# Optimization experiments

Hardware: AMD Instinct MI355X
Metric: run time of the kernel (lower is better)

Reference implementation:

```python
import jax, jax.numpy as jnp
import numpy as np

MODEL_DIM = 1024
HIDDEN = 2048
NUM_GROUPS = 2
EXPERTS_PER_GP = 4
NUM_EXPERTS = NUM_GROUPS * EXPERTS_PER_GP
TOP_K = 2
B, T = 2, 2048


def _swiglu(x):
    a, b = jnp.split(x, 2, axis=-1)
    return jax.nn.silu(a) * b


def setup_inputs() -> dict:
    key = jax.random.key(0)
    ks = jax.random.split(key, 7)
    s = 0.02  # init scale
    return {
        "x": jax.random.normal(ks[0], (B, T, MODEL_DIM), jnp.float32),
        # torch Linear weight layout [out_features, in_features]
        "w_in": jax.random.normal(ks[1], (HIDDEN * 2, MODEL_DIM), jnp.float32) * s,   # shared_in
        "w_out": jax.random.normal(ks[2], (MODEL_DIM, HIDDEN), jnp.float32) * s,      # shared_out
        "w1": jax.random.normal(ks[3], (HIDDEN * 2, MODEL_DIM), jnp.float32) * s,     # w1_shared
        "w2": jax.random.normal(ks[4], (NUM_EXPERTS, MODEL_DIM, HIDDEN), jnp.float32) * s,  # w2_expert stack
        "wg": jax.random.normal(ks[5], (NUM_GROUPS, MODEL_DIM), jnp.float32) * s,     # group_gate
        "we": jax.random.normal(ks[6], (NUM_EXPERTS, MODEL_DIM), jnp.float32) * s,    # expert_gate
        "gb": jnp.zeros((NUM_GROUPS,), jnp.float32),   # group_bias
        "eb": jnp.zeros((NUM_EXPERTS,), jnp.float32),  # expert_bias
    }


def reference(x, w_in, w_out, w1, w2, wg, we, gb, eb):
    Bs, Ts, C = x.shape
    S = Bs * Ts
    flat = x.reshape(S, C)

    # shared expert path
    shared = _swiglu(flat @ w_in.T) @ w_out.T                    # [S, C]

    # level-1: group gate (top-1)
    g_probs = jax.nn.softmax(flat @ wg.T + gb, axis=-1)          # [S, G]
    g_idx = jnp.argmax(g_probs, axis=-1)                         # [S]

    # level-2: expert gate masked to the chosen group
    e_logits = flat @ we.T + eb                                  # [S, E]
    egid = jnp.arange(NUM_EXPERTS) // EXPERTS_PER_GP             # expert -> group id
    masked = jnp.where(g_idx[:, None] == egid[None, :], e_logits, -jnp.inf)
    e_probs = jax.nn.softmax(masked, axis=-1)                    # zero outside group

    g_prob = jnp.take_along_axis(g_probs, g_idx[:, None], axis=1)  # [S, 1]
    p_expert = e_probs * g_prob                                  # [S, E]

    topv, topi = jax.lax.top_k(p_expert, TOP_K)                  # [S, k]

    # per-token per-expert combine weight (dense [S, E], rows k-sparse)
    w_se = jnp.zeros((S, NUM_EXPERTS), x.dtype).at[
        jnp.arange(S)[:, None], topi].add(topv)

    # w1 is shared across experts -> compute hidden once for all tokens
    h = _swiglu(flat @ w1.T)                                     # [S, H]

    # routed = sum_e w_se[:, e] * (h @ w2[e].T); scale commutes through linear
    routed = jnp.zeros_like(shared)
    for e in range(NUM_EXPERTS):  # small fixed expert count
        routed = routed + (h * w_se[:, e:e + 1]) @ w2[e].T

    return (shared + routed).reshape(Bs, Ts, C)
```

## Files before the change

### kernel.cpp

```cpp
#include <hip/hip_runtime.h>
#include <math.h>


#define C_DIM 1024
#define H_DIM 2048
#define S_TOK 4096

typedef _Float16 f16x8 __attribute__((ext_vector_type(8)));
typedef float f32x4 __attribute__((ext_vector_type(4)));

#define AS3(p) ((__attribute__((address_space(3))) void*)(p))
#define AS1c(p) ((const __attribute__((address_space(1))) void*)(p))

__global__ __launch_bounds__(256) void cvt_all(
    const float* __restrict__ x, const float* __restrict__ w_in,
    const float* __restrict__ w1, const float* __restrict__ w_out,
    const float* __restrict__ w2, _Float16* __restrict__ xh,
    _Float16* __restrict__ wprime, _Float16* __restrict__ wouth,
    _Float16* __restrict__ w2h) {
  int i = blockIdx.x * 256 + threadIdx.x;
  const float* s; _Float16* d; size_t soff, doff;
  if (i < 524288) { s = x; d = xh; soff = doff = (size_t)i; }
  else if (i < 1572864) {
    int n = i - 524288;
    int out_row = n >> 7, kc = n & 127;
    int wmat = out_row >> 12, r = out_row & 4095;
    int g = r >> 5, ii = r & 31;
    int src_row = (ii < 16) ? (g * 16 + ii) : (2048 + g * 16 + (ii - 16));
    s = wmat ? w1 : w_in; d = wprime;
    soff = (size_t)src_row * 128 + kc;
    doff = (size_t)n;
  } else if (i < 1835008) { int n = i - 1572864; s = w_out; d = wouth; soff = doff = (size_t)n; }
  else { int n = i - 1835008; s = w2; d = w2h; soff = doff = (size_t)n; }
  const float4* sp = reinterpret_cast<const float4*>(s) + soff * 2;
  float4 a = sp[0], b = sp[1];
  f16x8 h;
  h[0] = (_Float16)a.x; h[1] = (_Float16)a.y; h[2] = (_Float16)a.z; h[3] = (_Float16)a.w;
  h[4] = (_Float16)b.x; h[5] = (_Float16)b.y; h[6] = (_Float16)b.z; h[7] = (_Float16)b.w;
  reinterpret_cast<f16x8*>(d)[doff] = h;
}

__global__ __launch_bounds__(256) void gate_kernel(const float* __restrict__ x,
    const float* __restrict__ wg, const float* __restrict__ we,
    const float* __restrict__ gb, const float* __restrict__ eb,
    int* __restrict__ top2_e, float* __restrict__ top2_w) {
  const int lane = threadIdx.x & 63;
  const int token = blockIdx.x * 4 + (threadIdx.x >> 6);
  const float* xr = x + (size_t)token * C_DIM + lane * 16;
  float xv[16];
#pragma unroll
  for (int i = 0; i < 16; i += 4) {
    float4 t = *reinterpret_cast<const float4*>(xr + i);
    xv[i] = t.x; xv[i + 1] = t.y; xv[i + 2] = t.z; xv[i + 3] = t.w;
  }
  float dots[10];
#pragma unroll
  for (int g = 0; g < 10; ++g) {
    const float* wr = (g < 2 ? wg + (size_t)g * C_DIM : we + (size_t)(g - 2) * C_DIM) + lane * 16;
    float d = 0.f;
#pragma unroll
    for (int i = 0; i < 16; i += 4) {
      float4 t = *reinterpret_cast<const float4*>(wr + i);
      d += xv[i] * t.x + xv[i + 1] * t.y + xv[i + 2] * t.z + xv[i + 3] * t.w;
    }
#pragma unroll
    for (int off = 32; off > 0; off >>= 1) d += __shfl_xor(d, off);
    dots[g] = d;
  }
  if (lane != 0) return;
  float g0 = dots[0] + gb[0], g1 = dots[1] + gb[1];
  int gidx = (g0 >= g1) ? 0 : 1;
  float gm = fmaxf(g0, g1);
  float ex0 = expf(g0 - gm), ex1 = expf(g1 - gm);
  float gprob = (gidx == 0 ? ex0 : ex1) / (ex0 + ex1);
  const int base = gidx * 4;
  float el[4];
  float m = -1e30f;
#pragma unroll
  for (int jj = 0; jj < 4; ++jj) { el[jj] = dots[2 + base + jj] + eb[base + jj]; m = fmaxf(m, el[jj]); }
  float s = 0.f;
#pragma unroll
  for (int jj = 0; jj < 4; ++jj) { el[jj] = expf(el[jj] - m); s += el[jj]; }
  float p[8];
#pragma unroll
  for (int e = 0; e < 8; ++e) p[e] = 0.f;
#pragma unroll
  for (int jj = 0; jj < 4; ++jj) p[base + jj] = el[jj] / s * gprob;
  int i1 = 0; float v1 = -1.f;
#pragma unroll
  for (int e = 0; e < 8; ++e) if (p[e] > v1) { v1 = p[e]; i1 = e; }
  int i2 = -1; float v2 = -1.f;
#pragma unroll
  for (int e = 0; e < 8; ++e) if (e != i1 && p[e] > v2) { v2 = p[e]; i2 = e; }
  top2_e[token * 2] = i1;     top2_w[token * 2] = v1;
  top2_e[token * 2 + 1] = i2; top2_w[token * 2 + 1] = v2;
}

__global__ __launch_bounds__(256) void scanfill(const int* __restrict__ top2_e,
    const float* __restrict__ top2_w, int* __restrict__ offs_g,
    int* __restrict__ tok_list, float* __restrict__ scale_list,
    int* __restrict__ tok2slot) {
  __shared__ int cnt[8], offs[9], cur[8];
  const int tid = threadIdx.x;
  if (tid < 8) { cnt[tid] = 0; cur[tid] = 0; }
  __syncthreads();
  for (int i = tid; i < 2 * S_TOK; i += 256) atomicAdd(&cnt[top2_e[i]], 1);
  __syncthreads();
  if (tid == 0) {
    offs[0] = 0;
    for (int e = 0; e < 8; ++e) offs[e + 1] = offs[e] + cnt[e];
    for (int e = 0; e < 9; ++e) offs_g[e] = offs[e];
  }
  __syncthreads();
  for (int i = tid; i < 2 * S_TOK; i += 256) {
    int e = top2_e[i];
    int slot = atomicAdd(&cur[e], 1);
    int g = offs[e] + slot;
    tok_list[g] = i >> 1;
    scale_list[g] = top2_w[i];
    tok2slot[i] = g;
  }
}

__device__ __forceinline__ void stage_tile(_Float16* lds_, const _Float16* src,
                                           int ld, int tid) {
#pragma unroll
  for (int i = 0; i < 2; ++i) {
    int c = tid + i * 512;
    int row = c >> 3;
    int u = c & 7;
    const _Float16* g = src + (size_t)row * ld + ((u ^ (row & 7)) << 3);
    _Float16* l = lds_ + ((c & ~63) << 3);
    __builtin_amdgcn_global_load_lds(AS1c(g), AS3(l), 16, 0, 0);
  }
}

__device__ __forceinline__ f16x8 frag_ld(const _Float16* t, int row, int u) {
  return *reinterpret_cast<const f16x8*>(t + row * 64 + ((u ^ (row & 7)) << 3));
}

#define BAR __builtin_amdgcn_s_barrier()
#define LGKM0 do { asm volatile("s_waitcnt lgkmcnt(0)" ::: "memory"); \
                   __builtin_amdgcn_sched_barrier(0); } while (0)
#define PRI1 __builtin_amdgcn_s_setprio(1)
#define PRI0 __builtin_amdgcn_s_setprio(0)

#define STAGEA(h_, t_) do { \
  const _Float16* s_ = aS[h_] + (size_t)(t_) * 64; \
  _Float16* d_ = lds + ((t_) & 1) * 32768 + (h_) * 8192 + grp0; \
  __builtin_amdgcn_global_load_lds(AS1c(s_), AS3(d_), 16, 0, 0); \
  __builtin_amdgcn_global_load_lds(AS1c(s_ + 65536), AS3(d_ + 4096), 16, 0, 0); \
} while (0)
#define STAGEB(h_, t_) do { \
  const _Float16* s_ = bS[h_] + (size_t)(t_) * 64; \
  _Float16* d_ = lds + ((t_) & 1) * 32768 + 16384 + (h_) * 8192 + grp0; \
  __builtin_amdgcn_global_load_lds(AS1c(s_), AS3(d_), 16, 0, 0); \
  __builtin_amdgcn_global_load_lds(AS1c(s_ + 65536), AS3(d_ + 4096), 16, 0, 0); \
} while (0)

#define LDA(MB_) do { _Pragma("unroll") for (int mm = 0; mm < 4; ++mm) \
  { _Pragma("unroll") for (int ks = 0; ks < 2; ++ks) \
    af[mm][ks] = frag_ld(At, wm * 128 + (MB_) + mm * 16 + lr, ks * 4 + lq); } } while (0)
#define LDB(DST_, CB_) do { _Pragma("unroll") for (int nn = 0; nn < 2; ++nn) \
  { _Pragma("unroll") for (int ks = 0; ks < 2; ++ks) \
    DST_[nn][ks] = frag_ld(Bt, wn * 64 + (CB_) + nn * 16 + lr, ks * 4 + lq); } } while (0)
#define QUAD(MB_, BF_, NB_) do { \
  _Pragma("unroll") for (int ks = 0; ks < 2; ++ks) \
  _Pragma("unroll") for (int mm = 0; mm < 4; ++mm) \
  _Pragma("unroll") for (int nn = 0; nn < 2; ++nn) \
    acc[(MB_) + mm][(NB_) + nn] = __builtin_amdgcn_mfma_f32_16x16x32_f16( \
        af[mm][ks], BF_[nn][ks], acc[(MB_) + mm][(NB_) + nn], 0, 0, 0); \
} while (0)

__global__ __launch_bounds__(512, 2) void gemm_fused_swiglu(
    const _Float16* __restrict__ A, const _Float16* __restrict__ Wp,
    _Float16* __restrict__ H1, _Float16* __restrict__ H2) {
  __shared__ _Float16 lds[65536];
  const int tid = threadIdx.x;
  const int lane = tid & 63;
  const int wid = tid >> 6;
  const int wm = wid >> 2, wn = wid & 3;
  const int lr = lane & 15, lq = lane >> 4;

  const int bid = blockIdx.x;
  const int xcd = bid & 7, j = bid >> 3;
  const int nb = xcd * 4 + (j & 3);
  const int mb = j >> 2;
  const int row0 = mb * 256;
  const int colg0 = nb * 256;

  const int rA = tid >> 3, uA = tid & 7;
  const int grp0 = (tid & ~63) << 3;
  const int swz = (uA ^ (rA & 7)) << 3;
  const _Float16* aS[2];
  const _Float16* bS[2];
#pragma unroll
  for (int h = 0; h < 2; ++h) {
    aS[h] = A  + (size_t)(row0  + h * 128 + rA) * 1024 + swz;
    bS[h] = Wp + (size_t)(colg0 + h * 128 + rA) * 1024 + swz;
  }

  STAGEB(0, 0); STAGEB(1, 0); STAGEA(0, 0); STAGEA(1, 0);
  STAGEB(0, 1); STAGEB(1, 1); STAGEA(0, 1); STAGEA(1, 1);
  asm volatile("s_waitcnt vmcnt(8)" ::: "memory");
  BAR;

  f32x4 acc[8][4] = {};
  f16x8 af[4][2], bf[2][2], bf2[2][2];

  for (int t = 0; t < 16; ++t) {
    const _Float16* At = lds + (t & 1) * 32768;
    const _Float16* Bt = At + 16384;
    LDA(0); LDB(bf, 0);
    BAR; LGKM0; PRI1; QUAD(0, bf, 0); PRI0; BAR;
    LDB(bf2, 32);
    BAR; LGKM0; PRI1; QUAD(0, bf2, 2); PRI0; BAR;
    LDA(64);
    if (t < 14) { STAGEB(0, t + 2); STAGEB(1, t + 2); }
    BAR; LGKM0; PRI1; QUAD(4, bf, 0); PRI0; BAR;
    if (t < 14) { STAGEA(0, t + 2); STAGEA(1, t + 2); }
    BAR; PRI1; QUAD(4, bf2, 2); PRI0;
    if (t <= 13) { asm volatile("s_waitcnt vmcnt(8)" ::: "memory"); }
    else if (t == 14) { asm volatile("s_waitcnt vmcnt(0)" ::: "memory"); }
    BAR;
  }

  _Float16* Hd = (colg0 >= 4096) ? H2 : H1;
  const int col0 = colg0 & 4095;
  const int hbase = (col0 >> 1) + wn * 32 + lr;
#pragma unroll
  for (int mm = 0; mm < 8; ++mm)
#pragma unroll
    for (int np = 0; np < 2; ++np)
#pragma unroll
      for (int r = 0; r < 4; ++r) {
        float a = acc[mm][np * 2][r];
        float b = acc[mm][np * 2 + 1][r];
        float h = (a / (1.0f + expf(-a))) * b;
        int row = row0 + wm * 128 + mm * 16 + lq * 4 + r;
        Hd[(size_t)row * H_DIM + hbase + np * 16] = (_Float16)h;
      }
}

__global__ __launch_bounds__(512) void gemm_out(
    const _Float16* __restrict__ H1, const _Float16* __restrict__ H2,
    const _Float16* __restrict__ Wout, const _Float16* __restrict__ W2,
    const int* __restrict__ offs_g, const int* __restrict__ tok_list,
    const float* __restrict__ scale_list,
    float* __restrict__ out, _Float16* __restrict__ routed) {
  __shared__ _Float16 At[128 * 64];
  __shared__ _Float16 Bt[128 * 64];
  __shared__ float sse[128];
  const int tid = threadIdx.x;
  const int lane = tid & 63;
  const int wid = tid >> 6;
  const int wm = wid >> 2, wn = wid & 3;

  const int b = blockIdx.x;
  const bool shared_role = (b < 256);
  int rb, cb, offs_e = 0, n_e = 0;
  const _Float16* Bp;
  if (shared_role) {
    int x = b & 7, k = b >> 3;
    rb = x + (k >> 3) * 8; cb = k & 7;
    Bp = Wout;
  } else {
    int bp = b - 256;
    int e = bp & 7, k = bp >> 3;
    rb = k >> 3; cb = k & 7;
    offs_e = offs_g[e]; n_e = offs_g[e + 1] - offs_e;
    if (rb * 128 >= n_e) return;
    Bp = W2 + (size_t)e * C_DIM * H_DIM;
    if (tid < 128) {
      int lrr = rb * 128 + tid;
      sse[tid] = (lrr < n_e) ? scale_list[offs_e + lrr] : 0.f;
    }
  }

  const _Float16* aptr[2];
  _Float16* ldst[2];
#pragma unroll
  for (int i = 0; i < 2; ++i) {
    int c = tid + i * 512;
    int row = c >> 3, u = c & 7;
    int swz = (u ^ (row & 7)) << 3;
    const _Float16* rowbase;
    if (shared_role) {
      rowbase = H1 + (size_t)(rb * 128 + row) * H_DIM;
    } else {
      int lrr = rb * 128 + row;
      int gs = offs_e + (lrr < n_e ? lrr : n_e - 1);
      rowbase = H2 + (size_t)tok_list[gs] * H_DIM;
    }
    aptr[i] = rowbase + swz;
    ldst[i] = At + ((c & ~63) << 3);
  }

  f32x4 acc[4][2] = {};
  for (int kt = 0; kt < H_DIM; kt += 64) {
#pragma unroll
    for (int i = 0; i < 2; ++i)
      __builtin_amdgcn_global_load_lds(AS1c(aptr[i] + kt), AS3(ldst[i]), 16, 0, 0);
    stage_tile(Bt, Bp + (size_t)cb * 128 * H_DIM + kt, H_DIM, tid);
    __syncthreads();
#pragma unroll
    for (int ks = 0; ks < 2; ++ks) {
      const int u = (ks << 2) + (lane >> 4);
      f16x8 af[4], bfr[2];
#pragma unroll
      for (int m = 0; m < 4; ++m)
        af[m] = frag_ld(At, wm * 64 + m * 16 + (lane & 15), u);
#pragma unroll
      for (int n = 0; n < 2; ++n)
        bfr[n] = frag_ld(Bt, wn * 32 + n * 16 + (lane & 15), u);
#pragma unroll
      for (int m = 0; m < 4; ++m)
#pragma unroll
        for (int n = 0; n < 2; ++n)
          acc[m][n] = __builtin_amdgcn_mfma_f32_16x16x32_f16(af[m], bfr[n], acc[m][n], 0, 0, 0);
    }
    __syncthreads();
  }

#pragma unroll
  for (int m = 0; m < 4; ++m)
#pragma unroll
    for (int n = 0; n < 2; ++n)
#pragma unroll
      for (int r = 0; r < 4; ++r) {
        int rloc = wm * 64 + m * 16 + ((lane >> 4) << 2) + r;
        int col = cb * 128 + wn * 32 + n * 16 + (lane & 15);
        if (shared_role) {
          out[(size_t)(rb * 128 + rloc) * C_DIM + col] = acc[m][n][r];
        } else {
          int lrr = rb * 128 + rloc;
          if (lrr < n_e)
            routed[(size_t)(offs_e + lrr) * C_DIM + col] =
                (_Float16)(sse[rloc] * acc[m][n][r]);
        }
      }
}

__global__ __launch_bounds__(256) void combine_final(float* __restrict__ out,
    const _Float16* __restrict__ routed, const int* __restrict__ tok2slot) {
  const int t = blockIdx.x * 2 + (threadIdx.x >> 7);
  const int cp = (threadIdx.x & 127) << 3;
  const int s0 = tok2slot[t * 2], s1 = tok2slot[t * 2 + 1];
  f16x8 r0 = *reinterpret_cast<const f16x8*>(routed + (size_t)s0 * C_DIM + cp);
  f16x8 r1 = *reinterpret_cast<const f16x8*>(routed + (size_t)s1 * C_DIM + cp);
  float* op = out + (size_t)t * C_DIM + cp;
  float4 o0 = *reinterpret_cast<const float4*>(op);
  float4 o1 = *reinterpret_cast<const float4*>(op + 4);
  o0.x += (float)r0[0] + (float)r1[0];
  o0.y += (float)r0[1] + (float)r1[1];
  o0.z += (float)r0[2] + (float)r1[2];
  o0.w += (float)r0[3] + (float)r1[3];
  o1.x += (float)r0[4] + (float)r1[4];
  o1.y += (float)r0[5] + (float)r1[5];
  o1.z += (float)r0[6] + (float)r1[6];
  o1.w += (float)r0[7] + (float)r1[7];
  *reinterpret_cast<float4*>(op) = o0;
  *reinterpret_cast<float4*>(op + 4) = o1;
}

extern "C" void kernel_launch(void* const* d_in, const int* in_sizes, int n_in,
                              void* d_out, int out_size, void* d_ws, size_t ws_size,
                              hipStream_t stream) {
  const float* x     = (const float*)d_in[0];
  const float* w_in  = (const float*)d_in[1];
  const float* w_out = (const float*)d_in[2];
  const float* w1    = (const float*)d_in[3];
  const float* w2    = (const float*)d_in[4];
  const float* wg    = (const float*)d_in[5];
  const float* we    = (const float*)d_in[6];
  const float* gb    = (const float*)d_in[7];
  const float* eb    = (const float*)d_in[8];
  float* out = (float*)d_out;

  char* ws = (char*)d_ws;
  const size_t MB = 1u << 20;
  _Float16* xh     = (_Float16*)(ws + 0 * MB);
  _Float16* wprime = (_Float16*)(ws + 8 * MB);
  _Float16* routed = (_Float16*)(ws + 0 * MB);
  _Float16* wouth  = (_Float16*)(ws + 24 * MB);
  _Float16* w2h    = (_Float16*)(ws + 28 * MB);
  _Float16* H1     = (_Float16*)(ws + 60 * MB);
  _Float16* H2     = (_Float16*)(ws + 76 * MB);
  char* sm = ws + 92 * MB;
  int*   offs_g     = (int*)(sm);
  int*   top2_e     = (int*)(sm + 64);
  float* top2_w     = (float*)(sm + 64 + 32768);
  int*   tok_list   = (int*)(sm + 64 + 65536);
  float* scale_list = (float*)(sm + 64 + 98304);
  int*   tok2slot   = (int*)(sm + 64 + 131072);

  cvt_all<<<15360, 256, 0, stream>>>(x, w_in, w1, w_out, w2,
                                     xh, wprime, wouth, w2h);
  gate_kernel<<<1024, 256, 0, stream>>>(x, wg, we, gb, eb, top2_e, top2_w);
  scanfill<<<1, 256, 0, stream>>>(top2_e, top2_w, offs_g, tok_list,
                                  scale_list, tok2slot);

  gemm_fused_swiglu<<<512, 512, 0, stream>>>(xh, wprime, H1, H2);

  gemm_out<<<2304, 512, 0, stream>>>(H1, H2, wouth, w2h, offs_g, tok_list,
                                     scale_list, out, routed);
  combine_final<<<2048, 256, 0, stream>>>(out, routed, tok2slot);
}
```

Measured before the change: 345.2 us.

## Double-buffer gemm_out K-loop and stage swiglu output through LDS for coalesced stores

The output GEMM now keeps two LDS buffers per operand and prefetches the tile two steps ahead with global_load_lds. Fragment loads and MFMAs are interleaved with barriers and priority hints, so the global-to-LDS copies overlap with compute instead of sitting behind a full sync each iteration. The first GEMM's swiglu epilogue writes into a swizzled LDS tile and then issues 16-byte coalesced row stores instead of scattered 2-byte stores, and it uses the fast __expf. Block-index mapping for both roles changes, which can alter L2 reuse, and the doubled LDS footprint with launch bounds (512,4) may limit occupancy.

```diff
diff --git a/kernel.cpp b/kernel.cpp
--- a/kernel.cpp
+++ b/kernel.cpp
@@ -122,19 +122,6 @@
   }
 }
 
-__device__ __forceinline__ void stage_tile(_Float16* lds_, const _Float16* src,
-                                           int ld, int tid) {
-#pragma unroll
-  for (int i = 0; i < 2; ++i) {
-    int c = tid + i * 512;
-    int row = c >> 3;
-    int u = c & 7;
-    const _Float16* g = src + (size_t)row * ld + ((u ^ (row & 7)) << 3);
-    _Float16* l = lds_ + ((c & ~63) << 3);
-    __builtin_amdgcn_global_load_lds(AS1c(g), AS3(l), 16, 0, 0);
-  }
-}
-
 __device__ __forceinline__ f16x8 frag_ld(const _Float16* t, int row, int u) {
   return *reinterpret_cast<const f16x8*>(t + row * 64 + ((u ^ (row & 7)) << 3));
 }
@@ -226,8 +213,7 @@
   }
 
   _Float16* Hd = (colg0 >= 4096) ? H2 : H1;
-  const int col0 = colg0 & 4095;
-  const int hbase = (col0 >> 1) + wn * 32 + lr;
+  const int col0h = (colg0 & 4095) >> 1;
 #pragma unroll
   for (int mm = 0; mm < 8; ++mm)
 #pragma unroll
@@ -236,38 +222,52 @@
       for (int r = 0; r < 4; ++r) {
         float a = acc[mm][np * 2][r];
         float b = acc[mm][np * 2 + 1][r];
-        float h = (a / (1.0f + expf(-a))) * b;
-        int row = row0 + wm * 128 + mm * 16 + lq * 4 + r;
-        Hd[(size_t)row * H_DIM + hbase + np * 16] = (_Float16)h;
+        float h = (a / (1.0f + __expf(-a))) * b;
+        int row = wm * 128 + mm * 16 + lq * 4 + r;
+        int hcol = wn * 32 + np * 16 + lr;
+        lds[row * 128 + ((((hcol >> 3) ^ (row & 7)) << 3) | (hcol & 7))] = (_Float16)h;
       }
-}
-
-__global__ __launch_bounds__(512) void gemm_out(
+  __syncthreads();
+#pragma unroll
+  for (int i = 0; i < 8; ++i) {
+    int c = tid + i * 512;
+    int row = c >> 4, bblk = c & 15;
+    f16x8 v = *reinterpret_cast<const f16x8*>(lds + row * 128 + ((bblk ^ (row & 7)) << 3));
+    *reinterpret_cast<f16x8*>(Hd + (size_t)(row0 + row) * H_DIM + col0h + bblk * 8) = v;
+  }
+}
+
+#define OSTAGE(t_) do { int buf_ = ((t_) & 1) * 8192; \
+  _Pragma("unroll") for (int i_ = 0; i_ < 2; ++i_) { \
+    __builtin_amdgcn_global_load_lds(AS1c(aG[i_] + (size_t)(t_) * 64), AS3(aL[i_] + buf_), 16, 0, 0); \
+    __builtin_amdgcn_global_load_lds(AS1c(bG[i_] + (size_t)(t_) * 64), AS3(bL[i_] + buf_), 16, 0, 0); } \
+} while (0)
+
+__global__ __launch_bounds__(512, 4) void gemm_out(
     const _Float16* __restrict__ H1, const _Float16* __restrict__ H2,
     const _Float16* __restrict__ Wout, const _Float16* __restrict__ W2,
     const int* __restrict__ offs_g, const int* __restrict__ tok_list,
     const float* __restrict__ scale_list,
     float* __restrict__ out, _Float16* __restrict__ routed) {
-  __shared__ _Float16 At[128 * 64];
-  __shared__ _Float16 Bt[128 * 64];
+  __shared__ _Float16 AtF[2 * 128 * 64];
+  __shared__ _Float16 BtF[2 * 128 * 64];
   __shared__ float sse[128];
   const int tid = threadIdx.x;
   const int lane = tid & 63;
   const int wid = tid >> 6;
   const int wm = wid >> 2, wn = wid & 3;
+  const int lr = lane & 15, lq = lane >> 4;
 
   const int b = blockIdx.x;
   const bool shared_role = (b < 256);
   int rb, cb, offs_e = 0, n_e = 0;
   const _Float16* Bp;
   if (shared_role) {
-    int x = b & 7, k = b >> 3;
-    rb = x + (k >> 3) * 8; cb = k & 7;
+    rb = b >> 3; cb = b & 7;
     Bp = Wout;
   } else {
-    int bp = b - 256;
-    int e = bp & 7, k = bp >> 3;
-    rb = k >> 3; cb = k & 7;
+    int eb2 = b - 256;
+    int e = eb2 >> 8; rb = (eb2 >> 3) & 31; cb = eb2 & 7;
     offs_e = offs_g[e]; n_e = offs_g[e + 1] - offs_e;
     if (rb * 128 >= n_e) return;
     Bp = W2 + (size_t)e * C_DIM * H_DIM;
@@ -277,8 +277,10 @@
     }
   }
 
-  const _Float16* aptr[2];
-  _Float16* ldst[2];
+  const _Float16* aG[2];
+  const _Float16* bG[2];
+  _Float16* aL[2];
+  _Float16* bL[2];
 #pragma unroll
   for (int i = 0; i < 2; ++i) {
     int c = tid + i * 512;
@@ -292,34 +294,52 @@
       int gs = offs_e + (lrr < n_e ? lrr : n_e - 1);
       rowbase = H2 + (size_t)tok_list[gs] * H_DIM;
     }
-    aptr[i] = rowbase + swz;
-    ldst[i] = At + ((c & ~63) << 3);
-  }
+    aG[i] = rowbase + swz;
+    bG[i] = Bp + (size_t)(cb * 128 + row) * H_DIM + swz;
+    aL[i] = AtF + ((c & ~63) << 3);
+    bL[i] = BtF + ((c & ~63) << 3);
+  }
+
+  OSTAGE(0); OSTAGE(1);
+  asm volatile("s_waitcnt vmcnt(4)" ::: "memory");
+  BAR;
 
   f32x4 acc[4][2] = {};
-  for (int kt = 0; kt < H_DIM; kt += 64) {
-#pragma unroll
-    for (int i = 0; i < 2; ++i)
-      __builtin_amdgcn_global_load_lds(AS1c(aptr[i] + kt), AS3(ldst[i]), 16, 0, 0);
-    stage_tile(Bt, Bp + (size_t)cb * 128 * H_DIM + kt, H_DIM, tid);
-    __syncthreads();
-#pragma unroll
-    for (int ks = 0; ks < 2; ++ks) {
-      const int u = (ks << 2) + (lane >> 4);
-      f16x8 af[4], bfr[2];
-#pragma unroll
-      for (int m = 0; m < 4; ++m)
-        af[m] = frag_ld(At, wm * 64 + m * 16 + (lane & 15), u);
+  for (int t = 0; t < 32; ++t) {
+    const _Float16* Ab = AtF + (t & 1) * 8192;
+    const _Float16* Bb = BtF + (t & 1) * 8192;
+    f16x8 af[4][2], bfr[2][2];
+#pragma unroll
+    for (int m = 0; m < 4; ++m)
+#pragma unroll
+      for (int ks = 0; ks < 2; ++ks)
+        af[m][ks] = frag_ld(Ab, wm * 64 + m * 16 + lr, ks * 4 + lq);
+#pragma unroll
+    for (int n = 0; n < 2; ++n)
+#pragma unroll
+      for (int ks = 0; ks < 2; ++ks)
+        bfr[n][ks] = frag_ld(Bb, wn * 32 + n * 16 + lr, ks * 4 + lq);
+    BAR; LGKM0;
+    PRI1;
+#pragma unroll
+    for (int m = 0; m < 4; ++m)
 #pragma unroll
       for (int n = 0; n < 2; ++n)
-        bfr[n] = frag_ld(Bt, wn * 32 + n * 16 + (lane & 15), u);
-#pragma unroll
-      for (int m = 0; m < 4; ++m)
-#pragma unroll
-        for (int n = 0; n < 2; ++n)
-          acc[m][n] = __builtin_amdgcn_mfma_f32_16x16x32_f16(af[m], bfr[n], acc[m][n], 0, 0, 0);
-    }
-    __syncthreads();
+        acc[m][n] = __builtin_amdgcn_mfma_f32_16x16x32_f16(af[m][0], bfr[n][0], acc[m][n], 0, 0, 0);
+    PRI0;
+    BAR;
+    if (t < 30) OSTAGE(t + 2);
+    BAR;
+    PRI1;
+#pragma unroll
+    for (int m = 0; m < 4; ++m)
+#pragma unroll
+      for (int n = 0; n < 2; ++n)
+        acc[m][n] = __builtin_amdgcn_mfma_f32_16x16x32_f16(af[m][1], bfr[n][1], acc[m][n], 0, 0, 0);
+    PRI0;
+    if (t < 30) { asm volatile("s_waitcnt vmcnt(4)" ::: "memory"); }
+    else if (t == 30) { asm volatile("s_waitcnt vmcnt(0)" ::: "memory"); }
+    BAR;
   }
 
 #pragma unroll
@@ -328,8 +348,8 @@
     for (int n = 0; n < 2; ++n)
 #pragma unroll
       for (int r = 0; r < 4; ++r) {
-        int rloc = wm * 64 + m * 16 + ((lane >> 4) << 2) + r;
-        int col = cb * 128 + wn * 32 + n * 16 + (lane & 15);
+        int rloc = wm * 64 + m * 16 + (lq << 2) + r;
+        int col = cb * 128 + wn * 32 + n * 16 + lr;
         if (shared_role) {
           out[(size_t)(rb * 128 + rloc) * C_DIM + col] = acc[m][n][r];
         } else {
```

Measured after the change: 347.9 us. No clear change (+0.8%).
